# Kernel tuning notes

Hardware: AMD Instinct MI355X
Metric: run time of the kernel (lower is better)

Reference implementation:

```python
import jax, jax.numpy as jnp
import numpy as np

B, T, D, H = 32, 512, 1024, 1024


def setup_inputs() -> dict:
    key = jax.random.key(0)
    k1, k2, k3 = jax.random.split(key, 3)
    x = jax.random.normal(k1, (B, T, D), dtype=jnp.float32)
    c0 = jnp.zeros((B, H), dtype=jnp.float32)
    h0 = jnp.zeros((B, H), dtype=jnp.float32)
    # scale weights so gates do not saturate
    Wx = jax.random.normal(k2, (D, 4 * H), dtype=jnp.float32) * 0.05
    Wh = jax.random.normal(k3, (H, 4 * H), dtype=jnp.float32) * 0.05
    b = jnp.zeros((4 * H,), dtype=jnp.float32)
    return {"x": x, "c0": c0, "h0": h0, "Wx": Wx, "Wh": Wh, "b": b}


def reference(x, c0, h0, Wx, Wh, b):
    # Flax LSTMCell: gates = x @ Wx + h @ Wh + b, split into i,f,g,o.
    # Precompute the input projection for all timesteps (one big GEMM).
    xW = jnp.einsum('btd,dg->btg', x, Wx) + b  # [B,T,4H]

    def step(carry, xw_t):
        c, h = carry
        gates = xw_t + h @ Wh  # [B,4H]
        i, f, g, o = jnp.split(gates, 4, axis=-1)
        i = jax.nn.sigmoid(i)
        f = jax.nn.sigmoid(f)
        g = jnp.tanh(g)
        o = jax.nn.sigmoid(o)
        c_new = f * c + i * g
        h_new = o * jnp.tanh(c_new)
        return (c_new, h_new), h_new

    (cT, hT), ys = jax.lax.scan(step, (c0, h0), jnp.swapaxes(xW, 0, 1))
    outputs = jnp.swapaxes(ys, 0, 1)  # [B,T,H]
    return outputs, (cT, hT)
```

## Files before the change

### kernel.cpp

```cpp
#include <hip/hip_runtime.h>
#include <cstddef>

#define NB 32
#define NT 512
#define ND 1024
#define NH 1024
#define NG 4096
#define GRID 256

typedef unsigned short ushortT;
typedef __attribute__((ext_vector_type(8))) short short8;
typedef __attribute__((ext_vector_type(4))) float f32x4;
typedef __attribute__((ext_vector_type(4))) unsigned uint4v;

__device__ __forceinline__ ushortT f2bf(float f) {
    union { float f; unsigned u; } v; v.f = f;
    unsigned r = v.u + 0x7FFFu + ((v.u >> 16) & 1u);
    return (ushortT)(r >> 16);
}

__device__ __forceinline__ float pick4(float a0, float a1, float a2, float a3, int s) {
    float lo = (s & 1) ? a1 : a0;
    float hi = (s & 1) ? a3 : a2;
    return (s & 2) ? hi : lo;
}

__device__ __forceinline__ float fsigmoid(float x) {
    return __builtin_amdgcn_rcpf(1.f + __expf(-x));
}
__device__ __forceinline__ float ftanh(float x) {
    float xc = fminf(fmaxf(x, -15.f), 15.f);
    float e  = __expf(-2.f * xc);
    return (1.f - e) * __builtin_amdgcn_rcpf(1.f + e);
}

__global__ __launch_bounds__(256) void cast_bf16(const float* __restrict__ src,
                                                 ushortT* __restrict__ dst, int n4)
{
    int i = blockIdx.x * 256 + threadIdx.x;
    if (i < n4) {
        float4 v = ((const float4*)src)[i];
        ushort4 o;
        o.x = f2bf(v.x); o.y = f2bf(v.y); o.z = f2bf(v.z); o.w = f2bf(v.w);
        ((ushort4*)dst)[i] = o;
    }
}

__global__ __launch_bounds__(256) void transpose_cast(
    const float* __restrict__ src, ushortT* __restrict__ dst, int permute)
{
    __shared__ ushortT tile[64][66];
    const int c0 = blockIdx.x * 64, r0 = blockIdx.y * 64;
    const int cc = threadIdx.x & 63, rq = threadIdx.x >> 6;
    #pragma unroll
    for (int ps = 0; ps < 16; ++ps) {
        int r = ps * 4 + rq;
        tile[cc][r] = f2bf(src[(size_t)(r0 + r) * NG + c0 + cc]);
    }
    __syncthreads();
    #pragma unroll
    for (int ps = 0; ps < 16; ++ps) {
        int cl = ps * 4 + rq;
        int n  = c0 + cl;
        int drow = permute ? ((((n & 1023) >> 2) << 4) | ((n >> 10) << 2) | (n & 3))
                           : n;
        dst[(size_t)drow * 1024 + r0 + cc] = tile[cl][cc];
    }
}

__global__ __launch_bounds__(256) void gemm_xw_mfma(
    const ushortT* __restrict__ xb,
    const ushortT* __restrict__ wxT,
    const float* __restrict__ bias,
    float* __restrict__ XWP,
    int t0, int Tc, int tcsh)
{
    __shared__ ushortT As[128 * 32];
    __shared__ ushortT Bs[128 * 32];

    const int tid  = threadIdx.x;
    const int lane = tid & 63;
    const int wv   = tid >> 6;
    const int wr   = wv >> 1, wc = wv & 1;
    const int n0   = blockIdx.x * 128;
    const int m0   = blockIdx.y * 128;

    const int c1 = tid, c2 = tid + 256;
    const int rm1 = m0 + (c1 >> 2), rm2 = m0 + (c2 >> 2);
    const int xr1 = ((rm1 >> tcsh) * NT) + t0 + (rm1 & (Tc - 1));
    const int xr2 = ((rm2 >> tcsh) * NT) + t0 + (rm2 & (Tc - 1));
    const ushortT* ap1 = xb + (size_t)xr1 * ND + (c1 & 3) * 8;
    const ushortT* ap2 = xb + (size_t)xr2 * ND + (c2 & 3) * 8;
    const ushortT* bp1 = wxT + (size_t)(n0 + (c1 >> 2)) * ND + (c1 & 3) * 8;
    const ushortT* bp2 = wxT + (size_t)(n0 + (c2 >> 2)) * ND + (c2 & 3) * 8;

    f32x4 acc[4][4];
    #pragma unroll
    for (int m = 0; m < 4; ++m)
        #pragma unroll
        for (int n = 0; n < 4; ++n) acc[m][n] = (f32x4){0.f, 0.f, 0.f, 0.f};

    const int arow_base = (wr * 64 + (lane & 15)) * 32 + (lane >> 4) * 8;
    const int brow_base = (wc * 64 + (lane & 15)) * 32 + (lane >> 4) * 8;

    for (int k0 = 0; k0 < ND; k0 += 32) {
        short8 va1 = *(const short8*)(ap1 + k0);
        short8 va2 = *(const short8*)(ap2 + k0);
        short8 vb1 = *(const short8*)(bp1 + k0);
        short8 vb2 = *(const short8*)(bp2 + k0);
        __syncthreads();
        *(short8*)&As[c1 * 8] = va1;
        *(short8*)&As[c2 * 8] = va2;
        *(short8*)&Bs[c1 * 8] = vb1;
        *(short8*)&Bs[c2 * 8] = vb2;
        __syncthreads();
        short8 af[4], bf[4];
        #pragma unroll
        for (int m = 0; m < 4; ++m)
            af[m] = *(const short8*)&As[arow_base + m * 16 * 32];
        #pragma unroll
        for (int n = 0; n < 4; ++n)
            bf[n] = *(const short8*)&Bs[brow_base + n * 16 * 32];
        #pragma unroll
        for (int m = 0; m < 4; ++m)
            #pragma unroll
            for (int n = 0; n < 4; ++n)
                acc[m][n] = __builtin_amdgcn_mfma_f32_16x16x32_bf16(
                    af[m], bf[n], acc[m][n], 0, 0, 0);
    }

    #pragma unroll
    for (int n = 0; n < 4; ++n) {
        int col = n0 + wc * 64 + n * 16 + (lane & 15);
        int pc  = (((col & 1023) >> 2) << 4) | ((col >> 10) << 2) | (col & 3);
        float bs = bias[col];
        #pragma unroll
        for (int m = 0; m < 4; ++m) {
            #pragma unroll
            for (int r = 0; r < 4; ++r) {
                int rm = m0 + wr * 64 + m * 16 + (lane >> 4) * 4 + r;
                int b  = rm >> tcsh, tr = rm & (Tc - 1);
                XWP[((size_t)tr * NB + b) * NG + pc] = acc[m][n][r] + bs;
            }
        }
    }
}

__global__ __launch_bounds__(512) void lstm_persist(
    const float* __restrict__ XWP,
    const ushortT* __restrict__ whpT,
    unsigned* __restrict__ hb0,
    unsigned* __restrict__ hb1,
    const float* __restrict__ cinit,
    float* __restrict__ cT,
    float* __restrict__ out,
    float* __restrict__ hT,
    unsigned* __restrict__ flags,
    int t0, int Tc)
{
    __shared__ ushortT hs[16 * 1024];
    __shared__ float  red[8 * 16 * 17];

    const int tid  = threadIdx.x;
    const int lane = tid & 63;
    const int wv   = tid >> 6;
    const int grp  = blockIdx.x & 1;
    const int s    = blockIdx.x >> 1;

    const int ksp = wv >> 1;
    const int ct  = wv & 1;
    const int lo  = lane & 15;
    const int hi  = lane >> 4;

    const int rrow  = tid >> 5;
    const int col32 = tid & 31;
    const int rct   = col32 >> 4, rc16 = col32 & 15;
    const int gq    = (col32 >> 2) & 3;
    const int uu    = (col32 >> 4) * 4 + (col32 & 3);
    const int j     = s * 8 + uu;
    const int brow  = grp * 16 + rrow;

    short8 Bf[8];
    {
        const ushortT* bp = whpT + (size_t)(s * 32 + ct * 16 + lo) * NH
                                 + ksp * 256 + hi * 8;
        #pragma unroll
        for (int ks = 0; ks < 8; ++ks)
            Bf[ks] = *(const short8*)(bp + ks * 32);
    }

    float creg = cinit[(size_t)brow * NH + j];

    unsigned* const fl = flags + grp * 4 * 512;
    const int sub = s & 3;

    const int tend = t0 + Tc;
    for (int t = t0; t < tend; ++t) {
        const int trel = t - t0;
        const unsigned* hR = ((t & 1) ? hb0 : hb1) + grp * 8192;
        unsigned*       hW = ((t & 1) ? hb1 : hb0) + grp * 8192;

        #pragma unroll
        for (int u = 0; u < 4; ++u) {
            int d   = tid + u * 512;
            int row = d >> 7;
            int c16 = d & 127;
            const unsigned* sp = hR + row * 512 + c16 * 4;
            unsigned v0 = __hip_atomic_load(sp + 0, __ATOMIC_RELAXED, __HIP_MEMORY_SCOPE_AGENT);
            unsigned v1 = __hip_atomic_load(sp + 1, __ATOMIC_RELAXED, __HIP_MEMORY_SCOPE_AGENT);
            unsigned v2 = __hip_atomic_load(sp + 2, __ATOMIC_RELAXED, __HIP_MEMORY_SCOPE_AGENT);
            unsigned v3 = __hip_atomic_load(sp + 3, __ATOMIC_RELAXED, __HIP_MEMORY_SCOPE_AGENT);
            unsigned byte = (unsigned)row * 2048u
                          + (((unsigned)c16 * 16u) ^ (((unsigned)(row & 7)) << 4));
            *(uint4v*)((char*)hs + byte) = (uint4v){v0, v1, v2, v3};
        }
        float xv = XWP[((size_t)trel * NB + brow) * NG + s * 32 + col32];
        __syncthreads();

        f32x4 acc = (f32x4){0.f, 0.f, 0.f, 0.f};
        #pragma unroll
        for (int ks = 0; ks < 8; ++ks) {
            unsigned ab = (unsigned)lo * 2048u
                        + (((unsigned)(ksp * 512 + ks * 64 + hi * 16))
                           ^ (((unsigned)(lo & 7)) << 4));
            short8 a = *(const short8*)((char*)hs + ab);
            acc = __builtin_amdgcn_mfma_f32_16x16x32_bf16(a, Bf[ks], acc, 0, 0, 0);
        }
        #pragma unroll
        for (int r = 0; r < 4; ++r)
            red[wv * 272 + (hi * 4 + r) * 17 + lo] = acc[r];
        __syncthreads();

        float g = xv;
        #pragma unroll
        for (int kp = 0; kp < 4; ++kp)
            g += red[(kp * 2 + rct) * 272 + rrow * 17 + rc16];

        float g4  = __shfl_xor(g, 4);
        float g8  = __shfl_xor(g, 8);
        float g12 = __shfl_xor(g, 12);

        float gi = pick4(g, g4, g8, g12, gq);
        float gf = pick4(g, g4, g8, g12, gq ^ 1);
        float gg = pick4(g, g4, g8, g12, gq ^ 2);
        float go = pick4(g, g4, g8, g12, gq ^ 3);

        float iv = fsigmoid(gi);
        float fv = fsigmoid(gf);
        float gv = ftanh(gg);
        float ov = fsigmoid(go);
        float cn = fv * creg + iv * gv;
        float hn = ov * ftanh(cn);
        creg = cn;

        float ph = __shfl_xor(hn, 1);
        if (gq == 0) {
            if ((col32 & 1) == 0) {
                unsigned pair = (unsigned)f2bf(hn) | ((unsigned)f2bf(ph) << 16);
                __hip_atomic_store(&hW[rrow * 512 + (j >> 1)], pair,
                                   __ATOMIC_RELAXED, __HIP_MEMORY_SCOPE_AGENT);
                *(float2*)&out[((size_t)brow * NT + t) * NH + j] = make_float2(hn, ph);
            }
            if (t == NT - 1)   hT[(size_t)brow * NH + j] = hn;
            if (t == tend - 1) cT[(size_t)brow * NH + j] = cn;
        }

        if (t != tend - 1) {
            __syncthreads();
            if (tid == 0)
                __hip_atomic_fetch_add(&fl[sub * 512 + trel], 1u,
                                       __ATOMIC_RELAXED, __HIP_MEMORY_SCOPE_AGENT);
            if (tid < 4) {
                int it = 0;
                while (__hip_atomic_load(&fl[tid * 512 + trel], __ATOMIC_RELAXED,
                                         __HIP_MEMORY_SCOPE_AGENT) < 32u
                       && ++it < (1 << 18)) {}
            }
            __syncthreads();
        }
    }
}

extern "C" void kernel_launch(void* const* d_in, const int* in_sizes, int n_in,
                              void* d_out, int out_size, void* d_ws, size_t ws_size,
                              hipStream_t stream) {
    const float* x    = (const float*)d_in[0];
    const float* c0   = (const float*)d_in[1];
    const float* h0   = (const float*)d_in[2];
    const float* Wx   = (const float*)d_in[3];
    const float* Wh   = (const float*)d_in[4];
    const float* bias = (const float*)d_in[5];

    float* out = (float*)d_out;
    float* cT  = out + (size_t)NB * NT * NH;
    float* hT  = cT + (size_t)NB * NH;

    ushortT* xb   = (ushortT*)d_ws;
    ushortT* wxT  = xb  + (size_t)NB * NT * ND;
    ushortT* whpT = wxT + (size_t)NG * ND;
    unsigned* hb0 = (unsigned*)(whpT + (size_t)NG * NH);
    unsigned* hb1 = hb0 + NB * NH / 2;
    unsigned* flags = hb1 + NB * NH / 2;
    float*   xwp  = (float*)(flags + 2 * 4 * 512);

    const size_t fixed = ((size_t)NB * NT * ND + (size_t)NG * ND + (size_t)NG * NH
                          + 2 * NB * NH) * sizeof(ushortT) + 2 * 4 * 512 * 4 + 256;
    int Tc = 512;
    while (Tc > 4 && fixed + (size_t)NB * Tc * NG * sizeof(float) > ws_size)
        Tc >>= 1;
    int tcsh = 31 - __builtin_clz(Tc);

    cast_bf16<<<(NB * NT * ND / 4 + 255) / 256, 256, 0, stream>>>(x, xb, NB * NT * ND / 4);
    cast_bf16<<<(NB * NH / 4 + 255) / 256, 256, 0, stream>>>(h0, (ushortT*)hb1, NB * NH / 4);
    transpose_cast<<<dim3(64, 16), 256, 0, stream>>>(Wx, wxT, 0);
    transpose_cast<<<dim3(64, 16), 256, 0, stream>>>(Wh, whpT, 1);

    for (int t0 = 0; t0 < NT; t0 += Tc) {
        dim3 g(NG / 128, (NB * Tc) / 128);
        gemm_xw_mfma<<<g, 256, 0, stream>>>(xb, wxT, bias, xwp, t0, Tc, tcsh);
        hipMemsetAsync(flags, 0, 2 * 4 * 512 * sizeof(unsigned), stream);
        lstm_persist<<<GRID, 512, 0, stream>>>(
            xwp, whpT, hb0, hb1,
            (t0 == 0) ? c0 : (const float*)cT,
            cT, out, hT, flags, t0, Tc);
    }
}
```

Measured before the change: 2.310 ms.

## Store XW projection in bf16, split K across 8 waves, overlap loads with barrier

The input projection buffer is now written and read as bf16 instead of fp32, which halves its traffic and footprint and may allow larger time chunks. The GEMM uses global_load_lds to stage tiles directly into LDS. In the recurrent kernel each wave now loads only its own K slice of h and computes both column tiles over it, which removes one block barrier per step. The next step's XW value and the output store are issued after the flag increment so they overlap the inter-block spin wait. The cost is reduced precision of the pre-activations and an 8-way instead of 4-way LDS reduction.

New measurement: 2.096 ms. 9.3% less time.

```diff
diff --git a/kernel.cpp b/kernel.cpp
--- a/kernel.cpp
+++ b/kernel.cpp
@@ -13,10 +13,17 @@
 typedef __attribute__((ext_vector_type(4))) float f32x4;
 typedef __attribute__((ext_vector_type(4))) unsigned uint4v;
 
+#define GLL16(g, l) __builtin_amdgcn_global_load_lds(                      \
+    (const __attribute__((address_space(1))) void*)(g),                    \
+    (__attribute__((address_space(3))) void*)(l), 16, 0, 0)
+
 __device__ __forceinline__ ushortT f2bf(float f) {
     union { float f; unsigned u; } v; v.f = f;
     unsigned r = v.u + 0x7FFFu + ((v.u >> 16) & 1u);
     return (ushortT)(r >> 16);
+}
+__device__ __forceinline__ float bf2f(ushortT u) {
+    union { unsigned u; float f; } v; v.u = (unsigned)u << 16; return v.f;
 }
 
 __device__ __forceinline__ float pick4(float a0, float a1, float a2, float a3, int s) {
@@ -72,7 +79,7 @@
     const ushortT* __restrict__ xb,
     const ushortT* __restrict__ wxT,
     const float* __restrict__ bias,
-    float* __restrict__ XWP,
+    ushortT* __restrict__ XWPb,
     int t0, int Tc, int tcsh)
 {
     __shared__ ushortT As[128 * 32];
@@ -104,15 +111,11 @@
     const int brow_base = (wc * 64 + (lane & 15)) * 32 + (lane >> 4) * 8;
 
     for (int k0 = 0; k0 < ND; k0 += 32) {
-        short8 va1 = *(const short8*)(ap1 + k0);
-        short8 va2 = *(const short8*)(ap2 + k0);
-        short8 vb1 = *(const short8*)(bp1 + k0);
-        short8 vb2 = *(const short8*)(bp2 + k0);
         __syncthreads();
-        *(short8*)&As[c1 * 8] = va1;
-        *(short8*)&As[c2 * 8] = va2;
-        *(short8*)&Bs[c1 * 8] = vb1;
-        *(short8*)&Bs[c2 * 8] = vb2;
+        GLL16(ap1 + k0, &As[c1 * 8]);
+        GLL16(ap2 + k0, &As[c2 * 8]);
+        GLL16(bp1 + k0, &Bs[c1 * 8]);
+        GLL16(bp2 + k0, &Bs[c2 * 8]);
         __syncthreads();
         short8 af[4], bf[4];
         #pragma unroll
@@ -140,14 +143,14 @@
             for (int r = 0; r < 4; ++r) {
                 int rm = m0 + wr * 64 + m * 16 + (lane >> 4) * 4 + r;
                 int b  = rm >> tcsh, tr = rm & (Tc - 1);
-                XWP[((size_t)tr * NB + b) * NG + pc] = acc[m][n][r] + bs;
+                XWPb[((size_t)tr * NB + b) * NG + pc] = f2bf(acc[m][n][r] + bs);
             }
         }
     }
 }
 
 __global__ __launch_bounds__(512) void lstm_persist(
-    const float* __restrict__ XWP,
+    const ushortT* __restrict__ XWPb,
     const ushortT* __restrict__ whpT,
     unsigned* __restrict__ hb0,
     unsigned* __restrict__ hb1,
@@ -158,8 +161,8 @@
     unsigned* __restrict__ flags,
     int t0, int Tc)
 {
-    __shared__ ushortT hs[16 * 1024];
-    __shared__ float  red[8 * 16 * 17];
+    __shared__ ushortT hs[8 * 2048];
+    __shared__ float  red[16 * 272];
 
     const int tid  = threadIdx.x;
     const int lane = tid & 63;
@@ -167,10 +170,8 @@
     const int grp  = blockIdx.x & 1;
     const int s    = blockIdx.x >> 1;
 
-    const int ksp = wv >> 1;
-    const int ct  = wv & 1;
-    const int lo  = lane & 15;
-    const int hi  = lane >> 4;
+    const int lo = lane & 15;
+    const int hi = lane >> 4;
 
     const int rrow  = tid >> 5;
     const int col32 = tid & 31;
@@ -180,19 +181,20 @@
     const int j     = s * 8 + uu;
     const int brow  = grp * 16 + rrow;
 
-    short8 Bf[8];
-    {
-        const ushortT* bp = whpT + (size_t)(s * 32 + ct * 16 + lo) * NH
-                                 + ksp * 256 + hi * 8;
-        #pragma unroll
-        for (int ks = 0; ks < 8; ++ks)
-            Bf[ks] = *(const short8*)(bp + ks * 32);
-    }
+    short8 Bf[2][4];
+    #pragma unroll
+    for (int ct = 0; ct < 2; ++ct)
+        #pragma unroll
+        for (int ks = 0; ks < 4; ++ks)
+            Bf[ct][ks] = *(const short8*)(whpT
+                + (size_t)(s * 32 + ct * 16 + lo) * NH + wv * 128 + ks * 32 + hi * 8);
 
     float creg = cinit[(size_t)brow * NH + j];
 
     unsigned* const fl = flags + grp * 4 * 512;
     const int sub = s & 3;
+
+    ushortT xvr = XWPb[((size_t)0 * NB + brow) * NG + s * 32 + col32];
 
     const int tend = t0 + Tc;
     for (int t = t0; t < tend; ++t) {
@@ -202,39 +204,40 @@
 
         #pragma unroll
         for (int u = 0; u < 4; ++u) {
-            int d   = tid + u * 512;
-            int row = d >> 7;
-            int c16 = d & 127;
-            const unsigned* sp = hR + row * 512 + c16 * 4;
+            int cc  = lane + u * 64;
+            int row = cc >> 4, seg = cc & 15;
+            const unsigned* sp = hR + row * 512 + wv * 64 + seg * 4;
             unsigned v0 = __hip_atomic_load(sp + 0, __ATOMIC_RELAXED, __HIP_MEMORY_SCOPE_AGENT);
             unsigned v1 = __hip_atomic_load(sp + 1, __ATOMIC_RELAXED, __HIP_MEMORY_SCOPE_AGENT);
             unsigned v2 = __hip_atomic_load(sp + 2, __ATOMIC_RELAXED, __HIP_MEMORY_SCOPE_AGENT);
             unsigned v3 = __hip_atomic_load(sp + 3, __ATOMIC_RELAXED, __HIP_MEMORY_SCOPE_AGENT);
-            unsigned byte = (unsigned)row * 2048u
-                          + (((unsigned)c16 * 16u) ^ (((unsigned)(row & 7)) << 4));
+            unsigned byte = (unsigned)(wv * 4096 + row * 256)
+                          + (((unsigned)seg * 16u) ^ (((unsigned)(row & 7)) << 4));
             *(uint4v*)((char*)hs + byte) = (uint4v){v0, v1, v2, v3};
         }
-        float xv = XWP[((size_t)trel * NB + brow) * NG + s * 32 + col32];
+        float xv = bf2f(xvr);
+
+        f32x4 acc0 = (f32x4){0.f, 0.f, 0.f, 0.f};
+        f32x4 acc1 = (f32x4){0.f, 0.f, 0.f, 0.f};
+        #pragma unroll
+        for (int ks = 0; ks < 4; ++ks) {
+            unsigned ab = (unsigned)(wv * 4096 + lo * 256)
+                        + (((unsigned)(ks * 64 + hi * 16)) ^ (((unsigned)(lo & 7)) << 4));
+            short8 a = *(const short8*)((char*)hs + ab);
+            acc0 = __builtin_amdgcn_mfma_f32_16x16x32_bf16(a, Bf[0][ks], acc0, 0, 0, 0);
+            acc1 = __builtin_amdgcn_mfma_f32_16x16x32_bf16(a, Bf[1][ks], acc1, 0, 0, 0);
+        }
+        #pragma unroll
+        for (int r = 0; r < 4; ++r) {
+            red[(wv * 2 + 0) * 272 + (hi * 4 + r) * 17 + lo] = acc0[r];
+            red[(wv * 2 + 1) * 272 + (hi * 4 + r) * 17 + lo] = acc1[r];
+        }
         __syncthreads();
 
-        f32x4 acc = (f32x4){0.f, 0.f, 0.f, 0.f};
-        #pragma unroll
-        for (int ks = 0; ks < 8; ++ks) {
-            unsigned ab = (unsigned)lo * 2048u
-                        + (((unsigned)(ksp * 512 + ks * 64 + hi * 16))
-                           ^ (((unsigned)(lo & 7)) << 4));
-            short8 a = *(const short8*)((char*)hs + ab);
-            acc = __builtin_amdgcn_mfma_f32_16x16x32_bf16(a, Bf[ks], acc, 0, 0, 0);
-        }
-        #pragma unroll
-        for (int r = 0; r < 4; ++r)
-            red[wv * 272 + (hi * 4 + r) * 17 + lo] = acc[r];
-        __syncthreads();
-
         float g = xv;
         #pragma unroll
-        for (int kp = 0; kp < 4; ++kp)
-            g += red[(kp * 2 + rct) * 272 + rrow * 17 + rc16];
+        for (int w = 0; w < 8; ++w)
+            g += red[(w * 2 + rct) * 272 + rrow * 17 + rc16];
 
         float g4  = __shfl_xor(g, 4);
         float g8  = __shfl_xor(g, 8);
@@ -254,22 +257,21 @@
         creg = cn;
 
         float ph = __shfl_xor(hn, 1);
-        if (gq == 0) {
-            if ((col32 & 1) == 0) {
-                unsigned pair = (unsigned)f2bf(hn) | ((unsigned)f2bf(ph) << 16);
-                __hip_atomic_store(&hW[rrow * 512 + (j >> 1)], pair,
-                                   __ATOMIC_RELAXED, __HIP_MEMORY_SCOPE_AGENT);
-                *(float2*)&out[((size_t)brow * NT + t) * NH + j] = make_float2(hn, ph);
-            }
-            if (t == NT - 1)   hT[(size_t)brow * NH + j] = hn;
-            if (t == tend - 1) cT[(size_t)brow * NH + j] = cn;
-        }
+        const bool wlane = (gq == 0) && ((col32 & 1) == 0);
+        if (wlane) {
+            unsigned pair = (unsigned)f2bf(hn) | ((unsigned)f2bf(ph) << 16);
+            __hip_atomic_store(&hW[rrow * 512 + (j >> 1)], pair,
+                               __ATOMIC_RELAXED, __HIP_MEMORY_SCOPE_AGENT);
+        }
+        __syncthreads();
 
         if (t != tend - 1) {
-            __syncthreads();
             if (tid == 0)
                 __hip_atomic_fetch_add(&fl[sub * 512 + trel], 1u,
                                        __ATOMIC_RELAXED, __HIP_MEMORY_SCOPE_AGENT);
+            if (wlane)
+                *(float2*)&out[((size_t)brow * NT + t) * NH + j] = make_float2(hn, ph);
+            xvr = XWPb[((size_t)(trel + 1) * NB + brow) * NG + s * 32 + col32];
             if (tid < 4) {
                 int it = 0;
                 while (__hip_atomic_load(&fl[tid * 512 + trel], __ATOMIC_RELAXED,
@@ -277,6 +279,13 @@
                        && ++it < (1 << 18)) {}
             }
             __syncthreads();
+        } else {
+            if (gq == 0) {
+                if ((col32 & 1) == 0)
+                    *(float2*)&out[((size_t)brow * NT + t) * NH + j] = make_float2(hn, ph);
+                if (t == NT - 1) hT[(size_t)brow * NH + j] = hn;
+                cT[(size_t)brow * NH + j] = cn;
+            }
         }
     }
 }
@@ -301,12 +310,12 @@
     unsigned* hb0 = (unsigned*)(whpT + (size_t)NG * NH);
     unsigned* hb1 = hb0 + NB * NH / 2;
     unsigned* flags = hb1 + NB * NH / 2;
-    float*   xwp  = (float*)(flags + 2 * 4 * 512);
+    ushortT* xwpb = (ushortT*)(flags + 2 * 4 * 512);
 
     const size_t fixed = ((size_t)NB * NT * ND + (size_t)NG * ND + (size_t)NG * NH
                           + 2 * NB * NH) * sizeof(ushortT) + 2 * 4 * 512 * 4 + 256;
     int Tc = 512;
-    while (Tc > 4 && fixed + (size_t)NB * Tc * NG * sizeof(float) > ws_size)
+    while (Tc > 4 && fixed + (size_t)NB * Tc * NG * sizeof(ushortT) > ws_size)
         Tc >>= 1;
     int tcsh = 31 - __builtin_clz(Tc);
 
@@ -317,10 +326,10 @@
 
     for (int t0 = 0; t0 < NT; t0 += Tc) {
         dim3 g(NG / 128, (NB * Tc) / 128);
-        gemm_xw_mfma<<<g, 256, 0, stream>>>(xb, wxT, bias, xwp, t0, Tc, tcsh);
+        gemm_xw_mfma<<<g, 256, 0, stream>>>(xb, wxT, bias, xwpb, t0, Tc, tcsh);
         hipMemsetAsync(flags, 0, 2 * 4 * 512 * sizeof(unsigned), stream);
         lstm_persist<<<GRID, 512, 0, stream>>>(
-            xwp, whpT, hb0, hb1,
+            xwpb, whpT, hb0, hb1,
             (t0 == 0) ? c0 : (const float*)cT,
             cT, out, hT, flags, t0, Tc);
     }
```
